# Kernel optimization log

Hardware: AMD Instinct MI355X
Metric: run time of the kernel (lower is better)

Reference implementation:

```python
import jax, jax.numpy as jnp
import numpy as np
import math

D_MODEL = 256
NUM_HEADS = 8
K_NEIGHBORS = 16


def sine_pos_embedding(pos_xy, d_model):
    # Faithful to PositionalEncoding: pos_xy [B, N, 2] -> [B, N, d_model]
    half = d_model // 2
    dim_t = jnp.arange(half, dtype=jnp.float32)
    dim_t = 10000.0 ** (2.0 * jnp.floor(dim_t / 2.0) / half)
    recip = (2.0 * math.pi) / dim_t  # [half]
    px = pos_xy[:, :, 0, None] * recip  # [B, N, half]
    py = pos_xy[:, :, 1, None] * recip
    def interleave(p):
        s = jnp.sin(p[:, :, 0::2])
        c = jnp.cos(p[:, :, 1::2])
        return jnp.stack((s, c), axis=3).reshape(p.shape[0], p.shape[1], -1)
    return jnp.concatenate((interleave(py), interleave(px)), axis=2)


def knn_indices(pos, K, valid_mask):
    # Faithful to find_k_nearest_neighbors: cdist, mask invalid ROWS with +inf, topk smallest.
    # pos: [B, N, 3], valid_mask: [B, N] -> indices [B, N, K]
    sq = jnp.sum(pos * pos, axis=-1)  # [B, N]
    d2 = sq[:, :, None] + sq[:, None, :] - 2.0 * jnp.einsum('bnd,bmd->bnm', pos, pos)
    dist = jnp.sqrt(jnp.maximum(d2, 0.0))  # [B, N, N]
    INF = jnp.float32(np.inf)
    dist = jnp.where(valid_mask[:, :, None], dist, INF)  # torch masks rows via (~mask).unsqueeze(-1)
    _, idx = jax.lax.top_k(-dist, K)  # smallest distances
    return idx  # [B, N, K] int32


def setup_inputs() -> dict:
    key = jax.random.key(0)
    ks = jax.random.split(key, 8)
    B, N, D = 16, 1024, D_MODEL
    x = jax.random.normal(ks[0], (B, N, D), dtype=jnp.float32)
    x_pos = jax.random.normal(ks[1], (B, N, 3), dtype=jnp.float32) * 50.0
    x_mask = jax.random.bernoulli(ks[2], 0.9, (B, N))
    # guarantee at least one valid token per batch row (module asserts sum > 0)
    x_mask = x_mask.at[:, 0].set(True)
    scale = 1.0 / math.sqrt(D)
    Wq = jax.random.normal(ks[3], (D, D), dtype=jnp.float32) * scale
    Wk = jax.random.normal(ks[4], (D, D), dtype=jnp.float32) * scale
    Wv = jax.random.normal(ks[5], (D, D), dtype=jnp.float32) * scale
    Wo = jax.random.normal(ks[6], (D, D), dtype=jnp.float32) * scale
    return {"x": x, "x_pos": x_pos, "x_mask": x_mask,
            "Wq": Wq, "Wk": Wk, "Wv": Wv, "Wo": Wo}


def local_attention(x, pe, valid, idx, Wq, Wk, Wv, Wo):
    B, N, D = x.shape
    H = NUM_HEADS
    dh = D // H
    q = (x + pe) @ Wq  # [B, N, D]
    k = (x + pe) @ Wk
    v = x @ Wv
    # gather K neighbors per query: [B, N, K, D]
    gather = jax.vmap(lambda arr, ii: arr[ii])
    k_n = gather(k, idx)
    v_n = gather(v, idx)
    nbr_valid = gather(valid, idx)  # [B, N, K]
    q = q.reshape(B, N, H, dh)
    k_n = k_n.reshape(B, N, K_NEIGHBORS, H, dh)
    v_n = v_n.reshape(B, N, K_NEIGHBORS, H, dh)
    scores = jnp.einsum('bnhd,bnkhd->bnhk', q, k_n) / math.sqrt(dh)
    scores = jnp.where(nbr_valid[:, :, None, :], scores, jnp.float32(-1e9))
    attn = jax.nn.softmax(scores, axis=-1)
    out = jnp.einsum('bnhk,bnkhd->bnhd', attn, v_n).reshape(B, N, D)
    out = out @ Wo
    out = x + out  # residual
    # zero out invalid tokens, as ret_full_feature is zeros for invalid rows
    return jnp.where(valid[:, :, None], out, 0.0)


def reference(x, x_pos, x_mask, Wq, Wk, Wv, Wo):
    idx = knn_indices(x_pos, K_NEIGHBORS, x_mask)
    pe = sine_pos_embedding(x_pos[:, :, 0:2], D_MODEL)
    pe = jnp.where(x_mask[:, :, None], pe, 0.0)
    return local_attention(x, pe, x_mask, idx, Wq, Wk, Wv, Wo)
```

## Files before the change

### kernel.cpp

```cpp
#include <hip/hip_runtime.h>
#include <math.h>

#define BB 16
#define NN 1024
#define DD 256
#define HH 8
#define DHH 32
#define KNBR 16
#define MM (BB*NN)

typedef __attribute__((ext_vector_type(8))) short  bf16x8;
typedef __attribute__((ext_vector_type(4))) float  f32x4;
typedef __attribute__((ext_vector_type(2))) unsigned short u16x2;
typedef __attribute__((ext_vector_type(4))) unsigned short u16x4;

#define OFF_FLAG 0
#define OFF_XPE  ((size_t)256)
#define OFF_XBF  (OFF_XPE + (size_t)MM*DD*2)
#define OFF_WT   (OFF_XBF + (size_t)MM*DD*2)
#define OFF_Q    (OFF_WT  + (size_t)4*DD*DD*2)
#define OFF_K    (OFF_Q   + (size_t)MM*DD*2)
#define OFF_V    (OFF_K   + (size_t)MM*DD*2)
#define OFF_AO   OFF_XPE
#define OFF_IDX  (OFF_V   + (size_t)MM*DD*2)
#define WS_NEED  (OFF_IDX + (size_t)MM*KNBR*4)

__device__ __forceinline__ float bf2f(unsigned short u) {
    unsigned x = ((unsigned)u) << 16;
    return __builtin_bit_cast(float, x);
}
__device__ __forceinline__ unsigned short f2bf(float f) {
    unsigned x = __builtin_bit_cast(unsigned, f);
    unsigned r = (x + 0x7fffu + ((x >> 16) & 1u)) >> 16;
    return (unsigned short)r;
}
__device__ __forceinline__ int mbcnt64(unsigned long long b) {
    return __builtin_amdgcn_mbcnt_hi((unsigned)(b >> 32),
           __builtin_amdgcn_mbcnt_lo((unsigned)b, 0));
}

__device__ __forceinline__ int get_valid(const void* m, int i, int u8) {
    if (u8) return ((const unsigned char*)m)[i] != 0;
    return ((const unsigned*)m)[i] != 0u;
}

__global__ __launch_bounds__(256) void detect_kernel(
    const unsigned* __restrict__ mraw, int* __restrict__ flag) {
    __shared__ int s_u8, s_f32;
    if (threadIdx.x == 0) { s_u8 = 0; s_f32 = 0; }
    __syncthreads();
    int u8 = 0, f32 = 0;
    for (int i = threadIdx.x; i < 4096; i += 256) {
        unsigned w = mraw[i];
        if (w == 0x3f800000u) f32 = 1;
        else if (w > 1u) u8 = 1;
    }
    if (u8)  atomicOr(&s_u8, 1);
    if (f32) atomicOr(&s_f32, 1);
    __syncthreads();
    if (threadIdx.x == 0) *flag = (s_f32 ? 0 : (s_u8 ? 1 : 0));
}

__global__ __launch_bounds__(256, 8) void prep_fused(
    const float* __restrict__ xpos, int* __restrict__ idxout,
    const float* __restrict__ x, const void* __restrict__ mask,
    const int* __restrict__ flag,
    const float* __restrict__ Wq, const float* __restrict__ Wk,
    const float* __restrict__ Wv, const float* __restrict__ Wo,
    unsigned short* __restrict__ WT,
    unsigned short* __restrict__ xpebf, unsigned short* __restrict__ xbf) {
    __shared__ float4   sp[NN];
    __shared__ unsigned scand[4][64];
    int bid = blockIdx.x;
    int tid = threadIdx.x;

    if (bid >= 5120) {
        int pb = bid - 5120;
        int t = pb * 2 + (tid >> 7);
        int p = tid & 127;
        int u8 = *flag;
        int valid = get_valid(mask, t, u8);
        int half = p >> 6;
        int j = p & 63;
        float pos = xpos[(size_t)t*3 + (half ? 0 : 1)];
        float recip = 6.2831853071795864f * exp2f(-(float)j * 0.20762050593045952f);
        float th = pos * recip;
        float s, c;
        __sincosf(th, &s, &c);
        if (!valid) { s = 0.f; c = 0.f; }
        size_t o = (size_t)t*DD + half*128 + 2*j;
        float2 xv = *(const float2*)(x + o);
        u16x2 xb; xb[0] = f2bf(xv.x);     xb[1] = f2bf(xv.y);
        u16x2 xp; xp[0] = f2bf(xv.x + s); xp[1] = f2bf(xv.y + c);
        *(u16x2*)(xbf + o)   = xb;
        *(u16x2*)(xpebf + o) = xp;
        return;
    }
    if (bid >= 4096) {
        int g = bid - 4096;
        int wsel = g >> 8;
        int kk = g & 255;
        const float* W = (wsel == 0) ? Wq : (wsel == 1) ? Wk : (wsel == 2) ? Wv : Wo;
        WT[(size_t)wsel*65536 + (size_t)tid*256 + kk] = f2bf(W[(size_t)kk*256 + tid]);
        return;
    }

    int nblk = bid & 255;
    int b    = bid >> 8;
    for (int i = tid; i < NN; i += 256) {
        const float* p = xpos + ((size_t)b*NN + i)*3;
        float px = p[0], py = p[1], pz = p[2];
        sp[i] = make_float4(px, py, pz, px*px + py*py + pz*pz);
    }
    __syncthreads();
    int wave = tid >> 6, lane = tid & 63;
    int n = nblk * 4 + wave;
    float4 qp = sp[n];
    float d[16];
    #pragma unroll
    for (int t = 0; t < 16; ++t) {
        float4 pm = sp[lane + 64*t];
        float dot = qp.x*pm.x + qp.y*pm.y + qp.z*pm.z;
        float d2 = qp.w + pm.w - 2.f*dot;
        d[t] = fmaxf(d2, 0.f);
    }
    float lmin = d[0];
    #pragma unroll
    for (int t = 1; t < 16; ++t) lmin = fminf(lmin, d[t]);
    float xs = lmin;
    #pragma unroll
    for (int kk = 2; kk <= 64; kk <<= 1) {
        #pragma unroll
        for (int j = kk >> 1; j >= 1; j >>= 1) {
            float vv = __shfl_xor(xs, j);
            bool up = ((lane & kk) == 0);
            bool lower = ((lane & j) == 0);
            xs = (up == lower) ? fminf(xs, vv) : fmaxf(xs, vv);
        }
    }
    float tau = __shfl(xs, 15);
    int T = 0;
    #pragma unroll
    for (int t = 0; t < 16; ++t) T += (d[t] <= tau) ? 1 : 0;
    #pragma unroll
    for (int off = 1; off <= 32; off <<= 1) T += __shfl_xor(T, off);

    bool fast = (T <= 64);
    if (fast) {
        int base = 0;
        #pragma unroll
        for (int t = 0; t < 16; ++t) {
            bool c = (d[t] <= tau);
            unsigned long long bb = __ballot(c);
            if (c) scand[wave][base + mbcnt64(bb)] = __builtin_bit_cast(unsigned, d[t]);
            base += (int)__popcll(bb);
        }
    }
    __syncthreads();

    int out_base = (b*NN + n) * KNBR;
    if (fast) {
        unsigned key = (lane < T) ? scand[wave][lane] : 0xFFFFFFFFu;
        #pragma unroll
        for (int kk = 2; kk <= 64; kk <<= 1) {
            #pragma unroll
            for (int j = kk >> 1; j >= 1; j >>= 1) {
                unsigned vv = (unsigned)__shfl_xor((int)key, j);
                bool up = ((lane & kk) == 0);
                bool lower = ((lane & j) == 0);
                bool takemin = (up == lower);
                key = (takemin == (key < vv)) ? key : vv;
            }
        }
        unsigned tau2 = (unsigned)__shfl((int)key, 15);
        int c1 = (int)__popcll(__ballot(key < tau2));
        int lt_base = 0, eq_seen = 0;
        #pragma unroll
        for (int t = 0; t < 16; ++t) {
            unsigned du = __builtin_bit_cast(unsigned, d[t]);
            bool lt = du < tau2;
            bool eq = du == tau2;
            unsigned long long blt = __ballot(lt);
            unsigned long long beq = __ballot(eq);
            if (lt) idxout[out_base + lt_base + mbcnt64(blt)] = lane + 64*t;
            int er = eq_seen + mbcnt64(beq);
            if (eq && (c1 + er) < KNBR) idxout[out_base + c1 + er] = lane + 64*t;
            lt_base += (int)__popcll(blt);
            eq_seen += (int)__popcll(beq);
        }
    } else {
        #pragma unroll 1
        for (int it = 0; it < KNBR; ++it) {
            float bd = 3.4e38f; int bm = 1 << 30;
            #pragma unroll
            for (int t = 0; t < 16; ++t)
                if (d[t] < bd) { bd = d[t]; bm = lane + 64*t; }
            #pragma unroll
            for (int off = 32; off >= 1; off >>= 1) {
                float od = __shfl_xor(bd, off);
                int   om = __shfl_xor(bm, off);
                if (od < bd || (od == bd && om < bm)) { bd = od; bm = om; }
            }
            if (lane == 0) idxout[out_base + it] = bm;
            int sel = bm >> 6;
            int mine = ((bm & 63) == lane);
            #pragma unroll
            for (int t = 0; t < 16; ++t)
                if (mine && t == sel) d[t] = 3.4e38f;
        }
    }
}

template<int EPI>
__device__ __forceinline__ void gemm_mfma_core(
    const unsigned short* __restrict__ A, const unsigned short* __restrict__ BT,
    void* __restrict__ C, const float* __restrict__ resid,
    const void* __restrict__ mask, int u8, int bm, int bn, char* smem) {
    unsigned short (*As)[32] = (unsigned short (*)[32])smem;
    unsigned short (*Bs)[32] = (unsigned short (*)[32])(smem + 8192);
    int tid = threadIdx.x;
    int w = tid >> 6, l = tid & 63;
    int wr = w >> 1, wc = w & 1;

    f32x4 acc[4][4] = {};

    for (int kt = 0; kt < 8; ++kt) {
        #pragma unroll
        for (int j = 0; j < 2; ++j) {
            int c  = (w + j*4)*64 + l;
            int row = c >> 2;
            int cb  = (c & 3) * 16;
            const char* ga = (const char*)A + ((size_t)(bm + row)*256 + kt*32)*2 + cb;
            char* la = (char*)As + (size_t)(w + j*4)*1024;
            __builtin_amdgcn_global_load_lds(
                (const __attribute__((address_space(1))) unsigned*)ga,
                (__attribute__((address_space(3))) unsigned*)la, 16, 0, 0);
            const char* gb = (const char*)BT + ((size_t)(bn + row)*256 + kt*32)*2 + cb;
            char* lb = (char*)Bs + (size_t)(w + j*4)*1024;
            __builtin_amdgcn_global_load_lds(
                (const __attribute__((address_space(1))) unsigned*)gb,
                (__attribute__((address_space(3))) unsigned*)lb, 16, 0, 0);
        }
        __syncthreads();

        bf16x8 af[4], bfr[4];
        #pragma unroll
        for (int m = 0; m < 4; ++m)
            af[m] = *(const bf16x8*)&As[wr*64 + m*16 + (l & 15)][(l >> 4) * 8];
        #pragma unroll
        for (int n = 0; n < 4; ++n)
            bfr[n] = *(const bf16x8*)&Bs[wc*64 + n*16 + (l & 15)][(l >> 4) * 8];
        #pragma unroll
        for (int m = 0; m < 4; ++m)
            #pragma unroll
            for (int n = 0; n < 4; ++n)
                acc[m][n] = __builtin_amdgcn_mfma_f32_16x16x32_bf16(af[m], bfr[n], acc[m][n], 0, 0, 0);
        __syncthreads();
    }

    int colb = bn + wc*64 + (l & 15);
    #pragma unroll
    for (int m = 0; m < 4; ++m) {
        int row0 = bm + wr*64 + m*16 + (l >> 4)*4;
        #pragma unroll
        for (int r = 0; r < 4; ++r) {
            int row = row0 + r;
            int valid = 1;
            if (EPI) valid = get_valid(mask, row, u8);
            #pragma unroll
            for (int n = 0; n < 4; ++n) {
                int cc = colb + n*16;
                float val = acc[m][n][r];
                if (EPI) {
                    val = valid ? resid[(size_t)row*256 + cc] + val : 0.f;
                    ((float*)C)[(size_t)row*256 + cc] = val;
                } else {
                    ((unsigned short*)C)[(size_t)row*256 + cc] = f2bf(val);
                }
            }
        }
    }
}

__global__ __launch_bounds__(256) void gemm_qkv_mfma(
    const unsigned short* __restrict__ xpebf, const unsigned short* __restrict__ xbf,
    const unsigned short* __restrict__ WT,
    unsigned short* __restrict__ q, unsigned short* __restrict__ k,
    unsigned short* __restrict__ v) {
    __shared__ __align__(16) char smem[16384];
    int z = blockIdx.z;
    const unsigned short* A  = (z == 2) ? xbf : xpebf;
    const unsigned short* BT = WT + (size_t)z * 65536;
    unsigned short* C = (z == 0) ? q : (z == 1) ? k : v;
    gemm_mfma_core<0>(A, BT, C, nullptr, nullptr, 0, blockIdx.x*128, blockIdx.y*128, smem);
}

__global__ __launch_bounds__(256) void gemm_out_mfma(
    const unsigned short* __restrict__ aobf, const unsigned short* __restrict__ WT,
    const float* __restrict__ x, const void* __restrict__ mask,
    const int* __restrict__ flag, float* __restrict__ out) {
    __shared__ __align__(16) char smem[16384];
    int u8 = *flag;
    gemm_mfma_core<1>(aobf, WT + (size_t)3 * 65536, out, x, mask, u8,
                      blockIdx.x * 128, blockIdx.y * 128, smem);
}

__global__ __launch_bounds__(256) void attn_kernel(
    const unsigned short* __restrict__ q, const unsigned short* __restrict__ k,
    const unsigned short* __restrict__ v, const int* __restrict__ idx,
    const void* __restrict__ mask, const int* __restrict__ flag,
    unsigned short* __restrict__ aobf) {
    __shared__ int   s_j[4][16];
    __shared__ float s_w[4][16][8];
    int u8 = *flag;
    int wave = threadIdx.x >> 6, lane = threadIdx.x & 63;
    int cpx = gridDim.x >> 3;
    int sb = ((int)blockIdx.x & 7) * cpx + ((int)blockIdx.x >> 3);
    int t = sb * 4 + wave;
    int b = t >> 10;
    int sub = lane & 3, nbr = lane >> 2;
    int j = idx[(size_t)t*KNBR + nbr];
    if (lane < 16) s_j[wave][lane] = idx[(size_t)t*KNBR + lane];
    int nv = get_valid(mask, b*NN + j, u8);
    const unsigned short* qb = q + (size_t)t*DD;
    const unsigned short* kb = k + ((size_t)(b*NN + j))*DD;

    float w[8];
    #pragma unroll
    for (int h = 0; h < 8; ++h) {
        bf16x8 qv = *(const bf16x8*)(qb + h*32 + sub*8);
        bf16x8 kv = *(const bf16x8*)(kb + h*32 + sub*8);
        float acc = 0.f;
        #pragma unroll
        for (int e = 0; e < 8; ++e)
            acc += bf2f((unsigned short)qv[e]) * bf2f((unsigned short)kv[e]);
        acc += __shfl_xor(acc, 1);
        acc += __shfl_xor(acc, 2);
        float s = nv ? acc * 0.17677669529663688f : -1e9f;
        float m = s;
        #pragma unroll
        for (int off = 4; off <= 32; off <<= 1) m = fmaxf(m, __shfl_xor(m, off));
        float e = __expf(s - m);
        float sum = e;
        #pragma unroll
        for (int off = 4; off <= 32; off <<= 1) sum += __shfl_xor(sum, off);
        w[h] = e / sum;
    }
    if (sub == 0) {
        #pragma unroll
        for (int h = 0; h < 8; ++h) s_w[wave][nbr][h] = w[h];
    }
    __syncthreads();

    int c0 = lane * 4;
    int h = lane >> 3;
    float o0 = 0.f, o1 = 0.f, o2 = 0.f, o3 = 0.f;
    #pragma unroll
    for (int kk = 0; kk < 16; ++kk) {
        int jj = s_j[wave][kk];
        float wk = s_w[wave][kk][h];
        u16x4 vv = *(const u16x4*)(v + ((size_t)(b*NN + jj))*DD + c0);
        o0 += wk * bf2f(vv[0]);
        o1 += wk * bf2f(vv[1]);
        o2 += wk * bf2f(vv[2]);
        o3 += wk * bf2f(vv[3]);
    }
    u16x4 st;
    st[0] = f2bf(o0); st[1] = f2bf(o1); st[2] = f2bf(o2); st[3] = f2bf(o3);
    *(u16x4*)(aobf + (size_t)t*DD + c0) = st;
}

extern "C" void kernel_launch(void* const* d_in, const int* in_sizes, int n_in,
                              void* d_out, int out_size, void* d_ws, size_t ws_size,
                              hipStream_t stream) {
    const float* x    = (const float*)d_in[0];
    const float* xpos = (const float*)d_in[1];
    const void*  mask = d_in[2];
    const float* Wq   = (const float*)d_in[3];
    const float* Wk   = (const float*)d_in[4];
    const float* Wv   = (const float*)d_in[5];
    const float* Wo   = (const float*)d_in[6];
    float* out = (float*)d_out;
    char*  ws  = (char*)d_ws;
    if (ws_size < WS_NEED) return;

    int*            flag  = (int*)           (ws + OFF_FLAG);
    unsigned short* xpebf = (unsigned short*)(ws + OFF_XPE);
    unsigned short* xbf   = (unsigned short*)(ws + OFF_XBF);
    unsigned short* WT    = (unsigned short*)(ws + OFF_WT);
    unsigned short* q     = (unsigned short*)(ws + OFF_Q);
    unsigned short* k     = (unsigned short*)(ws + OFF_K);
    unsigned short* v     = (unsigned short*)(ws + OFF_V);
    unsigned short* aobf  = (unsigned short*)(ws + OFF_AO);
    int*            idx   = (int*)           (ws + OFF_IDX);

    detect_kernel<<<1, 256, 0, stream>>>((const unsigned*)mask, flag);
    prep_fused<<<13312, 256, 0, stream>>>(xpos, idx, x, mask, flag,
                                          Wq, Wk, Wv, Wo, WT, xpebf, xbf);
    gemm_qkv_mfma<<<dim3(128, 2, 3), 256, 0, stream>>>(xpebf, xbf, WT, q, k, v);
    attn_kernel<<<MM/4, 256, 0, stream>>>(q, k, v, idx, mask, flag, aobf);
    gemm_out_mfma<<<dim3(128, 2), 256, 0, stream>>>(aobf, WT, x, mask, flag, out);
}
```

Measured before the change: 86.85 us.

## Fold mask-format detection into prep kernel and widen GEMM tiles to full N

Mask-format detection moves into block 0 of the fused prep kernel, which removes one kernel launch. Because the flag is now written concurrently with the other prep blocks, positional-embedding zeroing for invalid rows is dropped. That is safe because invalid keys are masked in the scores and invalid output rows are zeroed. Both GEMMs switch to 128x256 tiles with 512 threads, so each A tile is loaded once per block instead of twice. The cost is fewer blocks (384 for QKV, 128 for the output projection) to spread across the CUs.

```diff
diff --git a/kernel.cpp b/kernel.cpp
--- a/kernel.cpp
+++ b/kernel.cpp
@@ -44,27 +44,10 @@
     return ((const unsigned*)m)[i] != 0u;
 }
 
-__global__ __launch_bounds__(256) void detect_kernel(
-    const unsigned* __restrict__ mraw, int* __restrict__ flag) {
-    __shared__ int s_u8, s_f32;
-    if (threadIdx.x == 0) { s_u8 = 0; s_f32 = 0; }
-    __syncthreads();
-    int u8 = 0, f32 = 0;
-    for (int i = threadIdx.x; i < 4096; i += 256) {
-        unsigned w = mraw[i];
-        if (w == 0x3f800000u) f32 = 1;
-        else if (w > 1u) u8 = 1;
-    }
-    if (u8)  atomicOr(&s_u8, 1);
-    if (f32) atomicOr(&s_f32, 1);
-    __syncthreads();
-    if (threadIdx.x == 0) *flag = (s_f32 ? 0 : (s_u8 ? 1 : 0));
-}
-
 __global__ __launch_bounds__(256, 8) void prep_fused(
     const float* __restrict__ xpos, int* __restrict__ idxout,
     const float* __restrict__ x, const void* __restrict__ mask,
-    const int* __restrict__ flag,
+    int* __restrict__ flag,
     const float* __restrict__ Wq, const float* __restrict__ Wk,
     const float* __restrict__ Wv, const float* __restrict__ Wo,
     unsigned short* __restrict__ WT,
@@ -74,12 +57,27 @@
     int bid = blockIdx.x;
     int tid = threadIdx.x;
 
-    if (bid >= 5120) {
-        int pb = bid - 5120;
+    if (bid == 0) {
+        __shared__ int s_u8, s_f32;
+        if (tid == 0) { s_u8 = 0; s_f32 = 0; }
+        __syncthreads();
+        int u8 = 0, f32 = 0;
+        const unsigned* mraw = (const unsigned*)mask;
+        for (int i = tid; i < 4096; i += 256) {
+            unsigned w = mraw[i];
+            if (w == 0x3f800000u) f32 = 1;
+            else if (w > 1u) u8 = 1;
+        }
+        if (u8)  atomicOr(&s_u8, 1);
+        if (f32) atomicOr(&s_f32, 1);
+        __syncthreads();
+        if (tid == 0) *flag = (s_f32 ? 0 : (s_u8 ? 1 : 0));
+        return;
+    }
+    if (bid >= 5121) {
+        int pb = bid - 5121;
         int t = pb * 2 + (tid >> 7);
         int p = tid & 127;
-        int u8 = *flag;
-        int valid = get_valid(mask, t, u8);
         int half = p >> 6;
         int j = p & 63;
         float pos = xpos[(size_t)t*3 + (half ? 0 : 1)];
@@ -87,7 +85,6 @@
         float th = pos * recip;
         float s, c;
         __sincosf(th, &s, &c);
-        if (!valid) { s = 0.f; c = 0.f; }
         size_t o = (size_t)t*DD + half*128 + 2*j;
         float2 xv = *(const float2*)(x + o);
         u16x2 xb; xb[0] = f2bf(xv.x);     xb[1] = f2bf(xv.y);
@@ -96,8 +93,8 @@
         *(u16x2*)(xpebf + o) = xp;
         return;
     }
-    if (bid >= 4096) {
-        int g = bid - 4096;
+    if (bid >= 4097) {
+        int g = bid - 4097;
         int wsel = g >> 8;
         int kk = g & 255;
         const float* W = (wsel == 0) ? Wq : (wsel == 1) ? Wk : (wsel == 2) ? Wv : Wo;
@@ -105,8 +102,9 @@
         return;
     }
 
-    int nblk = bid & 255;
-    int b    = bid >> 8;
+    int kb = bid - 1;
+    int nblk = kb & 255;
+    int b    = kb >> 8;
     for (int i = tid; i < NN; i += 256) {
         const float* p = xpos + ((size_t)b*NN + i)*3;
         float px = p[0], py = p[1], pz = p[2];
@@ -212,31 +210,33 @@
 }
 
 template<int EPI>
-__device__ __forceinline__ void gemm_mfma_core(
+__device__ __forceinline__ void gemm_mfma_core8(
     const unsigned short* __restrict__ A, const unsigned short* __restrict__ BT,
     void* __restrict__ C, const float* __restrict__ resid,
-    const void* __restrict__ mask, int u8, int bm, int bn, char* smem) {
+    const void* __restrict__ mask, int u8, int bm, char* smem) {
     unsigned short (*As)[32] = (unsigned short (*)[32])smem;
     unsigned short (*Bs)[32] = (unsigned short (*)[32])(smem + 8192);
     int tid = threadIdx.x;
     int w = tid >> 6, l = tid & 63;
-    int wr = w >> 1, wc = w & 1;
+    int wr = w >> 2, wc = w & 3;
 
     f32x4 acc[4][4] = {};
 
     for (int kt = 0; kt < 8; ++kt) {
-        #pragma unroll
-        for (int j = 0; j < 2; ++j) {
-            int c  = (w + j*4)*64 + l;
-            int row = c >> 2;
-            int cb  = (c & 3) * 16;
+        {
+            int row = tid >> 2, cb = (tid & 3) * 16;
             const char* ga = (const char*)A + ((size_t)(bm + row)*256 + kt*32)*2 + cb;
-            char* la = (char*)As + (size_t)(w + j*4)*1024;
+            char* la = (char*)As + (size_t)w*1024;
             __builtin_amdgcn_global_load_lds(
                 (const __attribute__((address_space(1))) unsigned*)ga,
                 (__attribute__((address_space(3))) unsigned*)la, 16, 0, 0);
-            const char* gb = (const char*)BT + ((size_t)(bn + row)*256 + kt*32)*2 + cb;
-            char* lb = (char*)Bs + (size_t)(w + j*4)*1024;
+        }
+        #pragma unroll
+        for (int j = 0; j < 2; ++j) {
+            int c = j*512 + tid;
+            int row = c >> 2, cb = (c & 3) * 16;
+            const char* gb = (const char*)BT + ((size_t)row*256 + kt*32)*2 + cb;
+            char* lb = (char*)Bs + (size_t)(j*8 + w)*1024;
             __builtin_amdgcn_global_load_lds(
                 (const __attribute__((address_space(1))) unsigned*)gb,
                 (__attribute__((address_space(3))) unsigned*)lb, 16, 0, 0);
@@ -258,7 +258,7 @@
         __syncthreads();
     }
 
-    int colb = bn + wc*64 + (l & 15);
+    int colb = wc*64 + (l & 15);
     #pragma unroll
     for (int m = 0; m < 4; ++m) {
         int row0 = bm + wr*64 + m*16 + (l >> 4)*4;
@@ -282,27 +282,27 @@
     }
 }
 
-__global__ __launch_bounds__(256) void gemm_qkv_mfma(
+__global__ __launch_bounds__(512) void gemm_qkv_mfma(
     const unsigned short* __restrict__ xpebf, const unsigned short* __restrict__ xbf,
     const unsigned short* __restrict__ WT,
     unsigned short* __restrict__ q, unsigned short* __restrict__ k,
     unsigned short* __restrict__ v) {
-    __shared__ __align__(16) char smem[16384];
-    int z = blockIdx.z;
+    __shared__ __align__(16) char smem[24576];
+    int z = blockIdx.y;
     const unsigned short* A  = (z == 2) ? xbf : xpebf;
     const unsigned short* BT = WT + (size_t)z * 65536;
     unsigned short* C = (z == 0) ? q : (z == 1) ? k : v;
-    gemm_mfma_core<0>(A, BT, C, nullptr, nullptr, 0, blockIdx.x*128, blockIdx.y*128, smem);
-}
-
-__global__ __launch_bounds__(256) void gemm_out_mfma(
+    gemm_mfma_core8<0>(A, BT, C, nullptr, nullptr, 0, blockIdx.x*128, smem);
+}
+
+__global__ __launch_bounds__(512) void gemm_out_mfma(
     const unsigned short* __restrict__ aobf, const unsigned short* __restrict__ WT,
     const float* __restrict__ x, const void* __restrict__ mask,
     const int* __restrict__ flag, float* __restrict__ out) {
-    __shared__ __align__(16) char smem[16384];
+    __shared__ __align__(16) char smem[24576];
     int u8 = *flag;
-    gemm_mfma_core<1>(aobf, WT + (size_t)3 * 65536, out, x, mask, u8,
-                      blockIdx.x * 128, blockIdx.y * 128, smem);
+    gemm_mfma_core8<1>(aobf, WT + (size_t)3 * 65536, out, x, mask, u8,
+                       blockIdx.x * 128, smem);
 }
 
 __global__ __launch_bounds__(256) void attn_kernel(
@@ -394,10 +394,9 @@
     unsigned short* aobf  = (unsigned short*)(ws + OFF_AO);
     int*            idx   = (int*)           (ws + OFF_IDX);
 
-    detect_kernel<<<1, 256, 0, stream>>>((const unsigned*)mask, flag);
-    prep_fused<<<13312, 256, 0, stream>>>(xpos, idx, x, mask, flag,
+    prep_fused<<<13313, 256, 0, stream>>>(xpos, idx, x, mask, flag,
                                           Wq, Wk, Wv, Wo, WT, xpebf, xbf);
-    gemm_qkv_mfma<<<dim3(128, 2, 3), 256, 0, stream>>>(xpebf, xbf, WT, q, k, v);
+    gemm_qkv_mfma<<<dim3(128, 3), 512, 0, stream>>>(xpebf, xbf, WT, q, k, v);
     attn_kernel<<<MM/4, 256, 0, stream>>>(q, k, v, idx, mask, flag, aobf);
-    gemm_out_mfma<<<dim3(128, 2), 256, 0, stream>>>(aobf, WT, x, mask, flag, out);
-}
+    gemm_out_mfma<<<128, 512, 0, stream>>>(aobf, WT, x, mask, flag, out);
+}
```

After: 88.52 us. Within noise of the previous version (+1.9%).
